# Kernel optimization log

Hardware: AMD Instinct MI355X
Metric: run time of the kernel (lower is better)

Reference implementation:

```python
import jax, jax.numpy as jnp
import numpy as np

IN0, OUT0 = 64, 64   # layer 0: input_size -> hidden
IN1, OUT1 = 64, 16   # layer 1: hidden -> output_size
H = 2                # subnetwork hidden width (subnetwork_shape=[2,2])
BATCH = 16384


def _make_layer_params(key, n_subnets):
    ks = jax.random.split(key, 6)
    s1 = 1.0  # fan_in=1
    s2 = 1.0 / np.sqrt(H)
    W1 = jax.random.uniform(ks[0], (n_subnets, H, 1), minval=-s1, maxval=s1)
    b1 = jax.random.uniform(ks[1], (n_subnets, H), minval=-s1, maxval=s1)
    W2 = jax.random.uniform(ks[2], (n_subnets, H, H), minval=-s2, maxval=s2)
    b2 = jax.random.uniform(ks[3], (n_subnets, H), minval=-s2, maxval=s2)
    W3 = jax.random.uniform(ks[4], (n_subnets, 1, H), minval=-s2, maxval=s2)
    b3 = jax.random.uniform(ks[5], (n_subnets, 1), minval=-s2, maxval=s2)
    return W1, b1, W2, b2, W3, b3


def setup_inputs() -> dict:
    key = jax.random.key(0)
    kx, k0, k1 = jax.random.split(key, 3)
    x = jax.random.normal(kx, (BATCH, IN0), dtype=jnp.float32)
    l0 = _make_layer_params(k0, IN0 * OUT0)
    l1 = _make_layer_params(k1, IN1 * OUT1)
    names = ['W1', 'b1', 'W2', 'b2', 'W3', 'b3']
    inp = {'x': x}
    for n, v in zip(names, l0):
        inp['l0_' + n] = v
    for n, v in zip(names, l1):
        inp['l1_' + n] = v
    return inp


def _kan_layer(x, in_size, out_size, W1, b1, W2, b2, W3, b3):
    # x: [B, in] -> x_expanded: [in*out, B, 1]; subnet n = i*out + o
    B = x.shape[0]
    xe = jnp.repeat(x.T, out_size, axis=0)[:, :, None]          # [N, B, 1]
    h = jax.nn.relu(jnp.einsum('nbi,nhi->nbh', xe, W1) + b1[:, None, :])  # [N, B, H]
    h = jax.nn.relu(jnp.einsum('nbh,nkh->nbk', h, W2) + b2[:, None, :])   # [N, B, H]
    o = jnp.einsum('nbk,nok->nbo', h, W3) + b3[:, None, :]                # [N, B, 1]
    o = o[..., 0].reshape(in_size, out_size, B).sum(axis=0)               # [out, B]
    return o.T                                                            # [B, out]


def reference(x, l0_W1, l0_b1, l0_W2, l0_b2, l0_W3, l0_b3,
              l1_W1, l1_b1, l1_W2, l1_b2, l1_W3, l1_b3):
    h = _kan_layer(x, IN0, OUT0, l0_W1, l0_b1, l0_W2, l0_b2, l0_W3, l0_b3)
    out = _kan_layer(h, IN1, OUT1, l1_W1, l1_b1, l1_W2, l1_b2, l1_W3, l1_b3)
    return out
```

## Files before the change

### kernel.cpp

```cpp
#include <hip/hip_runtime.h>


typedef float v2f __attribute__((ext_vector_type(2)));

#define BATCH 16384
#define TB    32

__global__ __launch_bounds__(512, 4) void kan_fused(
    const float* __restrict__ x,
    const float* __restrict__ A1, const float* __restrict__ a1,
    const float* __restrict__ A2, const float* __restrict__ a2,
    const float* __restrict__ A3, const float* __restrict__ a3,
    const float* __restrict__ B1, const float* __restrict__ c1,
    const float* __restrict__ B2, const float* __restrict__ c2,
    const float* __restrict__ B3, const float* __restrict__ c3,
    float* __restrict__ out)
{
    __shared__ float xs[64][36];
    __shared__ float hp[4][TB][64];
    __shared__ float ht[64][36];
    __shared__ float op[4][TB][16];

    const int t    = threadIdx.x;
    const int lane = t & 63;
    const int wave = t >> 6;
    const int iq   = wave & 3;
    const int bh   = wave >> 2;
    const int bB0  = blockIdx.x * TB;

    {
        const int k = t * 4;
        const float4 v = *(const float4*)(x + (long)bB0 * 64 + k);
        const int b = k >> 6, i = k & 63;
        xs[i][b] = v.x; xs[i + 1][b] = v.y; xs[i + 2][b] = v.z; xs[i + 3][b] = v.w;
    }
    __syncthreads();

    const v2f zz = {0.f, 0.f};
    const int boff = 16 * bh;

    {
        const int o  = lane;
        const int i0 = 16 * iq;

        auto ldw = [&](int i, v2f& w1, v2f& d1, float4& w2, v2f& d2, v2f& w3, float& b3v) {
            const int n = (i << 6) + o;
            w1  = *(const v2f*)(A1 + 2 * n);
            d1  = *(const v2f*)(a1 + 2 * n);
            w2  = *(const float4*)(A2 + 4 * n);
            d2  = *(const v2f*)(a2 + 2 * n);
            w3  = *(const v2f*)(A3 + 2 * n);
            b3v = a3[n];
        };

        float acc[16];
#pragma unroll
        for (int j = 0; j < 16; ++j) acc[j] = 0.f;
        float bsum = 0.f;

        v2f w1, d1, d2, w3; float4 w2; float b3v;
        ldw(i0, w1, d1, w2, d2, w3, b3v);

#pragma unroll 1
        for (int ii = 0; ii < 16; ++ii) {
            const int i = i0 + ii;
            v2f nw1, nd1, nd2, nw3; float4 nw2; float nb3;
            ldw(i0 + ((ii + 1) & 15), nw1, nd1, nw2, nd2, nw3, nb3);

            const float4 xv0 = *(const float4*)&xs[i][boff];
            const float4 xv1 = *(const float4*)&xs[i][boff + 4];
            const float4 xv2 = *(const float4*)&xs[i][boff + 8];
            const float4 xv3 = *(const float4*)&xs[i][boff + 12];
            const float4 xv[4] = {xv0, xv1, xv2, xv3};

            bsum += b3v;
            const v2f c0  = {w2.x, w2.z};
            const v2f c1v = {w2.y, w2.w};
#pragma unroll
            for (int j = 0; j < 16; ++j) {
                const float xb = ((const float*)xv)[j];
                const v2f xd = {xb, xb};
                v2f m = __builtin_elementwise_fma(xd, w1, d1);
                m = __builtin_elementwise_max(m, zz);
                const v2f mm0 = {m.x, m.x};
                const v2f mm1 = {m.y, m.y};
                v2f tt = __builtin_elementwise_fma(c1v, mm1, d2);
                tt = __builtin_elementwise_fma(c0, mm0, tt);
                tt = __builtin_elementwise_max(tt, zz);
                acc[j] = fmaf(w3.x, tt.x, fmaf(w3.y, tt.y, acc[j]));
            }
            w1 = nw1; d1 = nd1; w2 = nw2; d2 = nd2; w3 = nw3; b3v = nb3;
        }
#pragma unroll
        for (int j = 0; j < 16; ++j)
            hp[iq][boff + j][o] = acc[j] + bsum;
    }
    __syncthreads();

    for (int k = t; k < TB * 64; k += 512) {
        const int b = k >> 6, i = k & 63;
        ht[i][b] = hp[0][b][i] + hp[1][b][i] + hp[2][b][i] + hp[3][b][i];
    }
    __syncthreads();

    {
        const int o1 = lane & 15;
        const int ig = lane >> 4;
        const int i0 = 16 * iq + 4 * ig;

        auto ldw = [&](int i, v2f& w1, v2f& d1, float4& w2, v2f& d2, v2f& w3, float& b3v) {
            const int n = (i << 4) + o1;
            w1  = *(const v2f*)(B1 + 2 * n);
            d1  = *(const v2f*)(c1 + 2 * n);
            w2  = *(const float4*)(B2 + 4 * n);
            d2  = *(const v2f*)(c2 + 2 * n);
            w3  = *(const v2f*)(B3 + 2 * n);
            b3v = c3[n];
        };

        float acc[16];
#pragma unroll
        for (int j = 0; j < 16; ++j) acc[j] = 0.f;
        float bsum = 0.f;

        v2f w1, d1, d2, w3; float4 w2; float b3v;
        ldw(i0, w1, d1, w2, d2, w3, b3v);

#pragma unroll 1
        for (int ii = 0; ii < 4; ++ii) {
            const int i = i0 + ii;
            v2f nw1, nd1, nd2, nw3; float4 nw2; float nb3;
            ldw(i0 + ((ii + 1) & 3), nw1, nd1, nw2, nd2, nw3, nb3);

            const float4 hv0 = *(const float4*)&ht[i][boff];
            const float4 hv1 = *(const float4*)&ht[i][boff + 4];
            const float4 hv2 = *(const float4*)&ht[i][boff + 8];
            const float4 hv3 = *(const float4*)&ht[i][boff + 12];
            const float4 hv[4] = {hv0, hv1, hv2, hv3};

            bsum += b3v;
            const v2f c0  = {w2.x, w2.z};
            const v2f c1v = {w2.y, w2.w};
#pragma unroll
            for (int j = 0; j < 16; ++j) {
                const float hb = ((const float*)hv)[j];
                const v2f xd = {hb, hb};
                v2f m = __builtin_elementwise_fma(xd, w1, d1);
                m = __builtin_elementwise_max(m, zz);
                const v2f mm0 = {m.x, m.x};
                const v2f mm1 = {m.y, m.y};
                v2f tt = __builtin_elementwise_fma(c1v, mm1, d2);
                tt = __builtin_elementwise_fma(c0, mm0, tt);
                tt = __builtin_elementwise_max(tt, zz);
                acc[j] = fmaf(w3.x, tt.x, fmaf(w3.y, tt.y, acc[j]));
            }
            w1 = nw1; d1 = nd1; w2 = nw2; d2 = nd2; w3 = nw3; b3v = nb3;
        }

#pragma unroll
        for (int j = 0; j < 16; ++j) {
            float v = acc[j] + bsum;
            v += __shfl_xor(v, 16, 64);
            v += __shfl_xor(v, 32, 64);
            if (ig == 0) op[iq][boff + j][o1] = v;
        }
    }
    __syncthreads();

    if (t < 128) {
        const int f = t * 4;
        const float4 p0 = *(const float4*)(&op[0][0][0] + f);
        const float4 p1 = *(const float4*)(&op[1][0][0] + f);
        const float4 p2 = *(const float4*)(&op[2][0][0] + f);
        const float4 p3 = *(const float4*)(&op[3][0][0] + f);
        float4 r;
        r.x = p0.x + p1.x + p2.x + p3.x;
        r.y = p0.y + p1.y + p2.y + p3.y;
        r.z = p0.z + p1.z + p2.z + p3.z;
        r.w = p0.w + p1.w + p2.w + p3.w;
        *(float4*)(out + (long)bB0 * 16 + f) = r;
    }
}

extern "C" void kernel_launch(void* const* d_in, const int* in_sizes, int n_in,
                              void* d_out, int out_size, void* d_ws, size_t ws_size,
                              hipStream_t stream) {
    const float* x     = (const float*)d_in[0];
    const float* l0_W1 = (const float*)d_in[1];
    const float* l0_b1 = (const float*)d_in[2];
    const float* l0_W2 = (const float*)d_in[3];
    const float* l0_b2 = (const float*)d_in[4];
    const float* l0_W3 = (const float*)d_in[5];
    const float* l0_b3 = (const float*)d_in[6];
    const float* l1_W1 = (const float*)d_in[7];
    const float* l1_b1 = (const float*)d_in[8];
    const float* l1_W2 = (const float*)d_in[9];
    const float* l1_b2 = (const float*)d_in[10];
    const float* l1_W3 = (const float*)d_in[11];
    const float* l1_b3 = (const float*)d_in[12];

    float* outp = (float*)d_out;

    dim3 blk(512);
    dim3 grid(BATCH / TB);
    hipLaunchKernelGGL(kan_fused, grid, blk, 0, stream,
                       x,
                       l0_W1, l0_b1, l0_W2, l0_b2, l0_W3, l0_b3,
                       l1_W1, l1_b1, l1_W2, l1_b2, l1_W3, l1_b3,
                       outp);
}
```

Baseline: 103.0 us.

## Pre-transpose x in workspace and give each wave all batch rows with LDS atomics

Adds a separate transpose kernel that writes x as [64, BATCH] into the workspace. The fused kernel then has each wave cover all 32 batch rows for 8 input features, instead of 16 rows for 16 features, so each weight load is reused across twice as many rows and the x tile is no longer staged in shared memory. Partial sums are combined with shared-memory atomicAdd rather than per-wave partial buffers and a reduction pass. The costs are a second kernel launch, an extra global round trip for x, LDS atomic contention, and more accumulator registers under the 4-wave occupancy bound.

```diff
diff --git a/kernel.cpp b/kernel.cpp
--- a/kernel.cpp
+++ b/kernel.cpp
@@ -6,8 +6,35 @@
 #define BATCH 16384
 #define TB    32
 
-__global__ __launch_bounds__(512, 4) void kan_fused(
-    const float* __restrict__ x,
+__global__ __launch_bounds__(256) void xpose64(const float* __restrict__ x,
+                                               float* __restrict__ xT)
+{
+    __shared__ float tile[64][65];
+    const int t = threadIdx.x;
+    const long b0 = (long)blockIdx.x * 64;
+#pragma unroll
+    for (int p = 0; p < 4; ++p) {
+        const int idx = (p * 256 + t) * 4;
+        const int b = idx >> 6;
+        const int i = idx & 63;
+        const float4 v = *(const float4*)(x + (b0 + b) * 64 + i);
+        tile[i][b] = v.x; tile[i + 1][b] = v.y; tile[i + 2][b] = v.z; tile[i + 3][b] = v.w;
+    }
+    __syncthreads();
+#pragma unroll
+    for (int p = 0; p < 4; ++p) {
+        const int idx = (p * 256 + t) * 4;
+        const int i = idx >> 6;
+        const int b = idx & 63;
+        float4 v;
+        v.x = tile[i][b]; v.y = tile[i][b + 1]; v.z = tile[i][b + 2]; v.w = tile[i][b + 3];
+        *(float4*)(xT + (long)i * BATCH + b0 + b) = v;
+    }
+}
+
+template<bool XT>
+__global__ __launch_bounds__(512, 4) void kan_fused2(
+    const float* __restrict__ x, const float* __restrict__ xT,
     const float* __restrict__ A1, const float* __restrict__ a1,
     const float* __restrict__ A2, const float* __restrict__ a2,
     const float* __restrict__ A3, const float* __restrict__ a3,
@@ -16,32 +43,26 @@
     const float* __restrict__ B3, const float* __restrict__ c3,
     float* __restrict__ out)
 {
-    __shared__ float xs[64][36];
-    __shared__ float hp[4][TB][64];
-    __shared__ float ht[64][36];
-    __shared__ float op[4][TB][16];
+    __shared__ float ht[64][34];
+    __shared__ float op[TB][16];
 
     const int t    = threadIdx.x;
     const int lane = t & 63;
-    const int wave = t >> 6;
-    const int iq   = wave & 3;
-    const int bh   = wave >> 2;
+    const int w    = t >> 6;
     const int bB0  = blockIdx.x * TB;
 
     {
-        const int k = t * 4;
-        const float4 v = *(const float4*)(x + (long)bB0 * 64 + k);
-        const int b = k >> 6, i = k & 63;
-        xs[i][b] = v.x; xs[i + 1][b] = v.y; xs[i + 2][b] = v.z; xs[i + 3][b] = v.w;
+        float* hb = &ht[0][0];
+        for (int k = t; k < 64 * 34; k += 512) hb[k] = 0.f;
+        (&op[0][0])[t] = 0.f;
     }
     __syncthreads();
 
     const v2f zz = {0.f, 0.f};
-    const int boff = 16 * bh;
 
     {
         const int o  = lane;
-        const int i0 = 16 * iq;
+        const int i0 = 8 * w;
 
         auto ldw = [&](int i, v2f& w1, v2f& d1, float4& w2, v2f& d2, v2f& w3, float& b3v) {
             const int n = (i << 6) + o;
@@ -53,32 +74,43 @@
             b3v = a3[n];
         };
 
-        float acc[16];
-#pragma unroll
-        for (int j = 0; j < 16; ++j) acc[j] = 0.f;
+        float acc[TB];
+#pragma unroll
+        for (int j = 0; j < TB; ++j) acc[j] = 0.f;
         float bsum = 0.f;
 
         v2f w1, d1, d2, w3; float4 w2; float b3v;
         ldw(i0, w1, d1, w2, d2, w3, b3v);
 
 #pragma unroll 1
-        for (int ii = 0; ii < 16; ++ii) {
+        for (int ii = 0; ii < 8; ++ii) {
             const int i = i0 + ii;
             v2f nw1, nd1, nd2, nw3; float4 nw2; float nb3;
-            ldw(i0 + ((ii + 1) & 15), nw1, nd1, nw2, nd2, nw3, nb3);
-
-            const float4 xv0 = *(const float4*)&xs[i][boff];
-            const float4 xv1 = *(const float4*)&xs[i][boff + 4];
-            const float4 xv2 = *(const float4*)&xs[i][boff + 8];
-            const float4 xv3 = *(const float4*)&xs[i][boff + 12];
-            const float4 xv[4] = {xv0, xv1, xv2, xv3};
+            ldw(i0 + ((ii + 1) & 7), nw1, nd1, nw2, nd2, nw3, nb3);
+
+            float4 xq[8];
+            if constexpr (XT) {
+                const float* xr = xT + (long)i * BATCH + bB0;
+#pragma unroll
+                for (int q = 0; q < 8; ++q) xq[q] = *(const float4*)(xr + 4 * q);
+            } else {
+#pragma unroll
+                for (int q = 0; q < 8; ++q) {
+                    float4 v;
+                    v.x = x[(long)(bB0 + 4 * q + 0) * 64 + i];
+                    v.y = x[(long)(bB0 + 4 * q + 1) * 64 + i];
+                    v.z = x[(long)(bB0 + 4 * q + 2) * 64 + i];
+                    v.w = x[(long)(bB0 + 4 * q + 3) * 64 + i];
+                    xq[q] = v;
+                }
+            }
 
             bsum += b3v;
             const v2f c0  = {w2.x, w2.z};
             const v2f c1v = {w2.y, w2.w};
 #pragma unroll
-            for (int j = 0; j < 16; ++j) {
-                const float xb = ((const float*)xv)[j];
+            for (int j = 0; j < TB; ++j) {
+                const float xb = ((const float*)xq)[j];
                 const v2f xd = {xb, xb};
                 v2f m = __builtin_elementwise_fma(xd, w1, d1);
                 m = __builtin_elementwise_max(m, zz);
@@ -91,58 +123,41 @@
             }
             w1 = nw1; d1 = nd1; w2 = nw2; d2 = nd2; w3 = nw3; b3v = nb3;
         }
-#pragma unroll
-        for (int j = 0; j < 16; ++j)
-            hp[iq][boff + j][o] = acc[j] + bsum;
-    }
-    __syncthreads();
-
-    for (int k = t; k < TB * 64; k += 512) {
-        const int b = k >> 6, i = k & 63;
-        ht[i][b] = hp[0][b][i] + hp[1][b][i] + hp[2][b][i] + hp[3][b][i];
+
+#pragma unroll
+        for (int j = 0; j < TB; ++j)
+            atomicAdd(&ht[o][j], acc[j] + bsum);
     }
     __syncthreads();
 
     {
         const int o1 = lane & 15;
         const int ig = lane >> 4;
-        const int i0 = 16 * iq + 4 * ig;
-
-        auto ldw = [&](int i, v2f& w1, v2f& d1, float4& w2, v2f& d2, v2f& w3, float& b3v) {
+
+        float acc[TB];
+#pragma unroll
+        for (int j = 0; j < TB; ++j) acc[j] = 0.f;
+        float bsum = 0.f;
+
+#pragma unroll
+        for (int ii = 0; ii < 2; ++ii) {
+            const int i = 8 * w + 2 * ig + ii;
             const int n = (i << 4) + o1;
-            w1  = *(const v2f*)(B1 + 2 * n);
-            d1  = *(const v2f*)(c1 + 2 * n);
-            w2  = *(const float4*)(B2 + 4 * n);
-            d2  = *(const v2f*)(c2 + 2 * n);
-            w3  = *(const v2f*)(B3 + 2 * n);
-            b3v = c3[n];
-        };
-
-        float acc[16];
-#pragma unroll
-        for (int j = 0; j < 16; ++j) acc[j] = 0.f;
-        float bsum = 0.f;
-
-        v2f w1, d1, d2, w3; float4 w2; float b3v;
-        ldw(i0, w1, d1, w2, d2, w3, b3v);
-
-#pragma unroll 1
-        for (int ii = 0; ii < 4; ++ii) {
-            const int i = i0 + ii;
-            v2f nw1, nd1, nd2, nw3; float4 nw2; float nb3;
-            ldw(i0 + ((ii + 1) & 3), nw1, nd1, nw2, nd2, nw3, nb3);
-
-            const float4 hv0 = *(const float4*)&ht[i][boff];
-            const float4 hv1 = *(const float4*)&ht[i][boff + 4];
-            const float4 hv2 = *(const float4*)&ht[i][boff + 8];
-            const float4 hv3 = *(const float4*)&ht[i][boff + 12];
-            const float4 hv[4] = {hv0, hv1, hv2, hv3};
-
-            bsum += b3v;
+            const v2f w1    = *(const v2f*)(B1 + 2 * n);
+            const v2f d1    = *(const v2f*)(c1 + 2 * n);
+            const float4 w2 = *(const float4*)(B2 + 4 * n);
+            const v2f d2    = *(const v2f*)(c2 + 2 * n);
+            const v2f w3    = *(const v2f*)(B3 + 2 * n);
+            bsum += c3[n];
+
+            v2f hv[16];
+#pragma unroll
+            for (int q = 0; q < 16; ++q) hv[q] = *(const v2f*)(&ht[i][2 * q]);
+
             const v2f c0  = {w2.x, w2.z};
             const v2f c1v = {w2.y, w2.w};
 #pragma unroll
-            for (int j = 0; j < 16; ++j) {
+            for (int j = 0; j < TB; ++j) {
                 const float hb = ((const float*)hv)[j];
                 const v2f xd = {hb, hb};
                 v2f m = __builtin_elementwise_fma(xd, w1, d1);
@@ -154,31 +169,21 @@
                 tt = __builtin_elementwise_max(tt, zz);
                 acc[j] = fmaf(w3.x, tt.x, fmaf(w3.y, tt.y, acc[j]));
             }
-            w1 = nw1; d1 = nd1; w2 = nw2; d2 = nd2; w3 = nw3; b3v = nb3;
         }
 
 #pragma unroll
-        for (int j = 0; j < 16; ++j) {
+        for (int j = 0; j < TB; ++j) {
             float v = acc[j] + bsum;
             v += __shfl_xor(v, 16, 64);
             v += __shfl_xor(v, 32, 64);
-            if (ig == 0) op[iq][boff + j][o1] = v;
+            if (ig == 0) atomicAdd(&op[j][o1], v);
         }
     }
     __syncthreads();
 
     if (t < 128) {
-        const int f = t * 4;
-        const float4 p0 = *(const float4*)(&op[0][0][0] + f);
-        const float4 p1 = *(const float4*)(&op[1][0][0] + f);
-        const float4 p2 = *(const float4*)(&op[2][0][0] + f);
-        const float4 p3 = *(const float4*)(&op[3][0][0] + f);
-        float4 r;
-        r.x = p0.x + p1.x + p2.x + p3.x;
-        r.y = p0.y + p1.y + p2.y + p3.y;
-        r.z = p0.z + p1.z + p2.z + p3.z;
-        r.w = p0.w + p1.w + p2.w + p3.w;
-        *(float4*)(out + (long)bB0 * 16 + f) = r;
+        const float4 r = *(const float4*)(&op[0][0] + t * 4);
+        *(float4*)(out + (long)bB0 * 16 + t * 4) = r;
     }
 }
 
@@ -200,12 +205,25 @@
     const float* l1_b3 = (const float*)d_in[12];
 
     float* outp = (float*)d_out;
+    float* xT   = (float*)d_ws;
+    const bool use_xt = (d_ws != nullptr) &&
+                        (ws_size >= (size_t)BATCH * 64 * sizeof(float));
 
     dim3 blk(512);
     dim3 grid(BATCH / TB);
-    hipLaunchKernelGGL(kan_fused, grid, blk, 0, stream,
-                       x,
-                       l0_W1, l0_b1, l0_W2, l0_b2, l0_W3, l0_b3,
-                       l1_W1, l1_b1, l1_W2, l1_b2, l1_W3, l1_b3,
-                       outp);
+
+    if (use_xt) {
+        hipLaunchKernelGGL(xpose64, dim3(BATCH / 64), dim3(256), 0, stream, x, xT);
+        hipLaunchKernelGGL(kan_fused2<true>, grid, blk, 0, stream,
+                           x, xT,
+                           l0_W1, l0_b1, l0_W2, l0_b2, l0_W3, l0_b3,
+                           l1_W1, l1_b1, l1_W2, l1_b2, l1_W3, l1_b3,
+                           outp);
+    } else {
+        hipLaunchKernelGGL(kan_fused2<false>, grid, blk, 0, stream,
+                           x, x,
+                           l0_W1, l0_b1, l0_W2, l0_b2, l0_W3, l0_b3,
+                           l1_W1, l1_b1, l1_W2, l1_b2, l1_W3, l1_b3,
+                           outp);
+    }
 }
```

Measured after the change: 144.7 us. +40.5%, slower.

## Replace LDS partial-sum buffers with shared atomics and double-buffer weight loads

Applied to the files above, without the earlier changes.

The per-quarter partial buffers (hp, op) are replaced by shared-memory atomicAdd into zero-initialized ht and op. This removes one barrier and the separate reduction pass, and it shrinks LDS use. The main loops are unrolled by two with ping-pong weight and activation registers, so loads for the next input index overlap the current computation. The atomics add contention, make the float summation order nondeterministic, and the extra live registers may hurt occupancy.

```diff
diff --git a/kernel.cpp b/kernel.cpp
--- a/kernel.cpp
+++ b/kernel.cpp
@@ -6,7 +6,9 @@
 #define BATCH 16384
 #define TB    32
 
-__global__ __launch_bounds__(512, 4) void kan_fused(
+struct Wt { v2f w1, d1; float4 w2; v2f d2, w3; float b3; };
+
+__global__ __launch_bounds__(512, 4) void kan_fused5(
     const float* __restrict__ x,
     const float* __restrict__ A1, const float* __restrict__ a1,
     const float* __restrict__ A2, const float* __restrict__ a2,
@@ -17,9 +19,8 @@
     float* __restrict__ out)
 {
     __shared__ float xs[64][36];
-    __shared__ float hp[4][TB][64];
-    __shared__ float ht[64][36];
-    __shared__ float op[4][TB][16];
+    __shared__ float ht[64][34];
+    __shared__ float op[TB][16];
 
     const int t    = threadIdx.x;
     const int lane = t & 63;
@@ -27,8 +28,13 @@
     const int iq   = wave & 3;
     const int bh   = wave >> 2;
     const int bB0  = blockIdx.x * TB;
+    const int boff = 16 * bh;
 
     {
+        float* hb = &ht[0][0];
+        for (int k = t; k < 64 * 34; k += 512) hb[k] = 0.f;
+        (&op[0][0])[t] = 0.f;
+
         const int k = t * 4;
         const float4 v = *(const float4*)(x + (long)bB0 * 64 + k);
         const int b = k >> 6, i = k & 63;
@@ -37,20 +43,25 @@
     __syncthreads();
 
     const v2f zz = {0.f, 0.f};
-    const int boff = 16 * bh;
 
     {
         const int o  = lane;
         const int i0 = 16 * iq;
 
-        auto ldw = [&](int i, v2f& w1, v2f& d1, float4& w2, v2f& d2, v2f& w3, float& b3v) {
-            const int n = (i << 6) + o;
-            w1  = *(const v2f*)(A1 + 2 * n);
-            d1  = *(const v2f*)(a1 + 2 * n);
-            w2  = *(const float4*)(A2 + 4 * n);
-            d2  = *(const v2f*)(a2 + 2 * n);
-            w3  = *(const v2f*)(A3 + 2 * n);
-            b3v = a3[n];
+        auto ldw = [&](int i) {
+            Wt W; const int n = (i << 6) + o;
+            W.w1 = *(const v2f*)(A1 + 2 * n);
+            W.d1 = *(const v2f*)(a1 + 2 * n);
+            W.w2 = *(const float4*)(A2 + 4 * n);
+            W.d2 = *(const v2f*)(a2 + 2 * n);
+            W.w3 = *(const v2f*)(A3 + 2 * n);
+            W.b3 = a3[n];
+            return W;
+        };
+        auto ldx = [&](int i, float4* xv) {
+#pragma unroll
+            for (int q = 0; q < 4; ++q)
+                xv[q] = *(const float4*)&xs[i][boff + 4 * q];
         };
 
         float acc[16];
@@ -58,48 +69,42 @@
         for (int j = 0; j < 16; ++j) acc[j] = 0.f;
         float bsum = 0.f;
 
-        v2f w1, d1, d2, w3; float4 w2; float b3v;
-        ldw(i0, w1, d1, w2, d2, w3, b3v);
-
-#pragma unroll 1
-        for (int ii = 0; ii < 16; ++ii) {
-            const int i = i0 + ii;
-            v2f nw1, nd1, nd2, nw3; float4 nw2; float nb3;
-            ldw(i0 + ((ii + 1) & 15), nw1, nd1, nw2, nd2, nw3, nb3);
-
-            const float4 xv0 = *(const float4*)&xs[i][boff];
-            const float4 xv1 = *(const float4*)&xs[i][boff + 4];
-            const float4 xv2 = *(const float4*)&xs[i][boff + 8];
-            const float4 xv3 = *(const float4*)&xs[i][boff + 12];
-            const float4 xv[4] = {xv0, xv1, xv2, xv3};
-
-            bsum += b3v;
-            const v2f c0  = {w2.x, w2.z};
-            const v2f c1v = {w2.y, w2.w};
+        auto comp = [&](const Wt& W, const float4* xv) {
+            bsum += W.b3;
+            const v2f c0  = {W.w2.x, W.w2.z};
+            const v2f c1v = {W.w2.y, W.w2.w};
 #pragma unroll
             for (int j = 0; j < 16; ++j) {
                 const float xb = ((const float*)xv)[j];
                 const v2f xd = {xb, xb};
-                v2f m = __builtin_elementwise_fma(xd, w1, d1);
+                v2f m = __builtin_elementwise_fma(xd, W.w1, W.d1);
                 m = __builtin_elementwise_max(m, zz);
                 const v2f mm0 = {m.x, m.x};
                 const v2f mm1 = {m.y, m.y};
-                v2f tt = __builtin_elementwise_fma(c1v, mm1, d2);
+                v2f tt = __builtin_elementwise_fma(c1v, mm1, W.d2);
                 tt = __builtin_elementwise_fma(c0, mm0, tt);
                 tt = __builtin_elementwise_max(tt, zz);
-                acc[j] = fmaf(w3.x, tt.x, fmaf(w3.y, tt.y, acc[j]));
+                acc[j] = fmaf(W.w3.x, tt.x, fmaf(W.w3.y, tt.y, acc[j]));
             }
-            w1 = nw1; d1 = nd1; w2 = nw2; d2 = nd2; w3 = nw3; b3v = nb3;
+        };
+
+        Wt WA = ldw(i0), WB;
+        float4 XA[4], XB[4];
+        ldx(i0, XA);
+
+#pragma unroll 1
+        for (int ii = 0; ii < 16; ii += 2) {
+            WB = ldw(i0 + ((ii + 1) & 15));
+            ldx(i0 + ((ii + 1) & 15), XB);
+            comp(WA, XA);
+            WA = ldw(i0 + ((ii + 2) & 15));
+            ldx(i0 + ((ii + 2) & 15), XA);
+            comp(WB, XB);
         }
+
 #pragma unroll
         for (int j = 0; j < 16; ++j)
-            hp[iq][boff + j][o] = acc[j] + bsum;
-    }
-    __syncthreads();
-
-    for (int k = t; k < TB * 64; k += 512) {
-        const int b = k >> 6, i = k & 63;
-        ht[i][b] = hp[0][b][i] + hp[1][b][i] + hp[2][b][i] + hp[3][b][i];
+            atomicAdd(&ht[o][boff + j], acc[j] + bsum);
     }
     __syncthreads();
 
@@ -108,14 +113,20 @@
         const int ig = lane >> 4;
         const int i0 = 16 * iq + 4 * ig;
 
-        auto ldw = [&](int i, v2f& w1, v2f& d1, float4& w2, v2f& d2, v2f& w3, float& b3v) {
-            const int n = (i << 4) + o1;
-            w1  = *(const v2f*)(B1 + 2 * n);
-            d1  = *(const v2f*)(c1 + 2 * n);
-            w2  = *(const float4*)(B2 + 4 * n);
-            d2  = *(const v2f*)(c2 + 2 * n);
-            w3  = *(const v2f*)(B3 + 2 * n);
-            b3v = c3[n];
+        auto ldw = [&](int i) {
+            Wt W; const int n = (i << 4) + o1;
+            W.w1 = *(const v2f*)(B1 + 2 * n);
+            W.d1 = *(const v2f*)(c1 + 2 * n);
+            W.w2 = *(const float4*)(B2 + 4 * n);
+            W.d2 = *(const v2f*)(c2 + 2 * n);
+            W.w3 = *(const v2f*)(B3 + 2 * n);
+            W.b3 = c3[n];
+            return W;
+        };
+        auto ldh = [&](int i, v2f* hv) {
+#pragma unroll
+            for (int q = 0; q < 8; ++q)
+                hv[q] = *(const v2f*)&ht[i][boff + 2 * q];
         };
 
         float acc[16];
@@ -123,38 +134,37 @@
         for (int j = 0; j < 16; ++j) acc[j] = 0.f;
         float bsum = 0.f;
 
-        v2f w1, d1, d2, w3; float4 w2; float b3v;
-        ldw(i0, w1, d1, w2, d2, w3, b3v);
-
-#pragma unroll 1
-        for (int ii = 0; ii < 4; ++ii) {
-            const int i = i0 + ii;
-            v2f nw1, nd1, nd2, nw3; float4 nw2; float nb3;
-            ldw(i0 + ((ii + 1) & 3), nw1, nd1, nw2, nd2, nw3, nb3);
-
-            const float4 hv0 = *(const float4*)&ht[i][boff];
-            const float4 hv1 = *(const float4*)&ht[i][boff + 4];
-            const float4 hv2 = *(const float4*)&ht[i][boff + 8];
-            const float4 hv3 = *(const float4*)&ht[i][boff + 12];
-            const float4 hv[4] = {hv0, hv1, hv2, hv3};
-
-            bsum += b3v;
-            const v2f c0  = {w2.x, w2.z};
-            const v2f c1v = {w2.y, w2.w};
+        auto comp = [&](const Wt& W, const v2f* hv) {
+            bsum += W.b3;
+            const v2f c0  = {W.w2.x, W.w2.z};
+            const v2f c1v = {W.w2.y, W.w2.w};
 #pragma unroll
             for (int j = 0; j < 16; ++j) {
                 const float hb = ((const float*)hv)[j];
                 const v2f xd = {hb, hb};
-                v2f m = __builtin_elementwise_fma(xd, w1, d1);
+                v2f m = __builtin_elementwise_fma(xd, W.w1, W.d1);
                 m = __builtin_elementwise_max(m, zz);
                 const v2f mm0 = {m.x, m.x};
                 const v2f mm1 = {m.y, m.y};
-                v2f tt = __builtin_elementwise_fma(c1v, mm1, d2);
+                v2f tt = __builtin_elementwise_fma(c1v, mm1, W.d2);
                 tt = __builtin_elementwise_fma(c0, mm0, tt);
                 tt = __builtin_elementwise_max(tt, zz);
-                acc[j] = fmaf(w3.x, tt.x, fmaf(w3.y, tt.y, acc[j]));
+                acc[j] = fmaf(W.w3.x, tt.x, fmaf(W.w3.y, tt.y, acc[j]));
             }
-            w1 = nw1; d1 = nd1; w2 = nw2; d2 = nd2; w3 = nw3; b3v = nb3;
+        };
+
+        Wt WA = ldw(i0), WB;
+        v2f HA[8], HB[8];
+        ldh(i0, HA);
+
+#pragma unroll 1
+        for (int ii = 0; ii < 4; ii += 2) {
+            WB = ldw(i0 + ((ii + 1) & 3));
+            ldh(i0 + ((ii + 1) & 3), HB);
+            comp(WA, HA);
+            WA = ldw(i0 + ((ii + 2) & 3));
+            ldh(i0 + ((ii + 2) & 3), HA);
+            comp(WB, HB);
         }
 
 #pragma unroll
@@ -162,23 +172,14 @@
             float v = acc[j] + bsum;
             v += __shfl_xor(v, 16, 64);
             v += __shfl_xor(v, 32, 64);
-            if (ig == 0) op[iq][boff + j][o1] = v;
+            if (ig == 0) atomicAdd(&op[boff + j][o1], v);
         }
     }
     __syncthreads();
 
     if (t < 128) {
-        const int f = t * 4;
-        const float4 p0 = *(const float4*)(&op[0][0][0] + f);
-        const float4 p1 = *(const float4*)(&op[1][0][0] + f);
-        const float4 p2 = *(const float4*)(&op[2][0][0] + f);
-        const float4 p3 = *(const float4*)(&op[3][0][0] + f);
-        float4 r;
-        r.x = p0.x + p1.x + p2.x + p3.x;
-        r.y = p0.y + p1.y + p2.y + p3.y;
-        r.z = p0.z + p1.z + p2.z + p3.z;
-        r.w = p0.w + p1.w + p2.w + p3.w;
-        *(float4*)(out + (long)bB0 * 16 + f) = r;
+        const float4 r = *(const float4*)(&op[0][0] + t * 4);
+        *(float4*)(out + (long)bB0 * 16 + t * 4) = r;
     }
 }
 
@@ -203,7 +204,8 @@
 
     dim3 blk(512);
     dim3 grid(BATCH / TB);
-    hipLaunchKernelGGL(kan_fused, grid, blk, 0, stream,
+
+    hipLaunchKernelGGL(kan_fused5, grid, blk, 0, stream,
                        x,
                        l0_W1, l0_b1, l0_W2, l0_b2, l0_W3, l0_b3,
                        l1_W1, l1_b1, l1_W2, l1_b2, l1_W3, l1_b3,
```

Measured after the change: 143.7 us. 39.5% more time.
